# Optimization experiments

Hardware: AMD Instinct MI355X
Metric: run time of the kernel (lower is better)

## Reference

```python
import jax, jax.numpy as jnp
import numpy as np


def _mlp2(x, W1, b1, W2, b2):
    # ReluMLP with two Dense layers: relu between layers, linear output
    return jax.nn.relu(x @ W1 + b1) @ W2 + b2


def setup_inputs() -> dict:
    key = jax.random.key(0)
    N, NP, DIN, D = 100000, 25000, 16, 64
    E, EDS, EP, EUS = 1_600_000, 800_000, 400_000, 200_000
    L = 8  # number of message-passing layers actually used
    ks = iter(jax.random.split(key, 40))
    nrm = lambda shape: jax.random.normal(next(ks), shape, jnp.float32) * 0.05
    ri = lambda n, hi: jax.random.randint(next(ks), (n,), 0, hi)
    return dict(
        x=jax.random.normal(next(ks), (N, DIN), jnp.float32),
        We1=nrm((DIN, D)), be1=jnp.zeros((D,), jnp.float32),
        We2=nrm((D, D)), be2=jnp.zeros((D,), jnp.float32),
        Wm1=nrm((L, D, D)), bm1=jnp.zeros((L, D), jnp.float32),
        Wm2=nrm((L, D, D)), bm2=jnp.zeros((L, D), jnp.float32),
        Wn1=nrm((L, 2 * D, D)), bn1=jnp.zeros((L, D), jnp.float32),
        Wn2=nrm((L, D, D)), bn2=jnp.zeros((L, D), jnp.float32),
        Wd1=nrm((D, D)), bd1=jnp.zeros((D,), jnp.float32),
        Wd2=nrm((D, 2)), bd2=jnp.zeros((2,), jnp.float32),
        s_fine=ri(E, N), r_fine=ri(E, N),
        s_ds=ri(EDS, N), r_ds=ri(EDS, N),
        s_p=ri(EP, NP), r_p=ri(EP, NP),
        s_us=ri(EUS, NP), r_us=ri(EUS, NP),
        uppool=ri(N, NP), downpool=ri(NP, NP),
    )


def reference(x, We1, be1, We2, be2, Wm1, bm1, Wm2, bm2, Wn1, bn1, Wn2, bn2,
              Wd1, bd1, Wd2, bd2, s_fine, r_fine, s_ds, r_ds, s_p, r_p,
              s_us, r_us, uppool, downpool):
    def mp(l, h, s, r, n):
        # LinearMessagePassingLayer: message MLP on sender feats,
        # sum-scatter to receivers (mean_aggr=False), node MLP on [h, aggr]
        msg = _mlp2(h[s], Wm1[l], bm1[l], Wm2[l], bm2[l])          # [E, D]
        aggr = jax.ops.segment_sum(msg, r, num_segments=n)          # [n, D]
        return _mlp2(jnp.concatenate([h, aggr], -1),
                     Wn1[l], bn1[l], Wn2[l], bn2[l])                # [n, D]

    N = x.shape[0]
    NP = downpool.shape[0]
    # encode
    h = _mlp2(x, We1, be1, We2, be2)                                 # [N, D]
    h = mp(0, h, s_fine, r_fine, N)
    h = mp(1, h, s_fine, r_fine, N)
    skip = h
    # Downsample: gather by uppool idx, MP on downsampling graph, select pooled
    g = mp(2, h[uppool], s_ds, r_ds, N)                              # [N, D]
    hp = g[downpool]                                                 # [NP, D]
    # bottleneck
    hp = mp(3, hp, s_p, r_p, NP)
    hp = mp(4, hp, s_p, r_p, NP)
    # Upsample: gather by downpool idx, MP on upsampling graph, select by uppool
    g = mp(5, hp[downpool], s_us, r_us, NP)                          # [NP, D]
    h = g[uppool]                                                    # [N, D]
    # decode with skip connections
    h = mp(6, h, s_fine, r_fine, N) + skip
    h = mp(7, h, s_fine, r_fine, N) + skip
    return _mlp2(h, Wd1, bd1, Wd2, bd2)                              # [N, 2]
```

## Files before the change

kernel.cpp:

```cpp
#include <hip/hip_runtime.h>

#define WG 256

#define MLP_FMA16(ACC, A, W) do { \
    ACC[0][0]=fmaf(A.x,W.x,ACC[0][0]); ACC[0][1]=fmaf(A.x,W.y,ACC[0][1]); \
    ACC[0][2]=fmaf(A.x,W.z,ACC[0][2]); ACC[0][3]=fmaf(A.x,W.w,ACC[0][3]); \
    ACC[1][0]=fmaf(A.y,W.x,ACC[1][0]); ACC[1][1]=fmaf(A.y,W.y,ACC[1][1]); \
    ACC[1][2]=fmaf(A.y,W.z,ACC[1][2]); ACC[1][3]=fmaf(A.y,W.w,ACC[1][3]); \
    ACC[2][0]=fmaf(A.z,W.x,ACC[2][0]); ACC[2][1]=fmaf(A.z,W.y,ACC[2][1]); \
    ACC[2][2]=fmaf(A.z,W.z,ACC[2][2]); ACC[2][3]=fmaf(A.z,W.w,ACC[2][3]); \
    ACC[3][0]=fmaf(A.w,W.x,ACC[3][0]); ACC[3][1]=fmaf(A.w,W.y,ACC[3][1]); \
    ACC[3][2]=fmaf(A.w,W.z,ACC[3][2]); ACC[3][3]=fmaf(A.w,W.w,ACC[3][3]); \
} while (0)

template<int DINA, bool HAS_B, bool HAS_SKIP, bool GATHER_A,
         int MSG_DOUT, bool PARTIAL_MSG, bool WRITE_OUT1>
__global__ __launch_bounds__(WG)
void mlp2_fused(const float* __restrict__ inA, const int* __restrict__ gidxA,
                const float* __restrict__ inB,
                const float* __restrict__ W1, const float* __restrict__ b1,
                const float* __restrict__ W2, const float* __restrict__ b2,
                const float* __restrict__ skip, float* __restrict__ out1,
                const float* __restrict__ M1, const float* __restrict__ mb1,
                const float* __restrict__ M2, const float* __restrict__ mb2,
                float* __restrict__ outM, int msgN, int n)
{
    constexpr int XP = 68;
    __shared__ __align__(16) float sXT[64][XP];
    __shared__ __align__(16) float sW[64 * 64];
    __shared__ float sb[128];
    __shared__ float sW2d[128];
    __shared__ float sb2d[2];

    const int tid = threadIdx.x;
    const int tx = tid & 15, ty = tid >> 4;
    const int c0 = tx * 4, r0 = ty * 4;
    const int row0 = blockIdx.x * 64;
    const int lrow = tid & 63;
    const int kq0 = (tid >> 6) * 4;

    for (int i = tid * 4; i < DINA * 64; i += WG * 4)
        *(float4*)&sW[i] = *(const float4*)&W1[i];
    if (tid < 64) sb[tid] = b1[tid];
    else if (tid < 128) sb[tid] = b2[tid - 64];

    {
        const int rg = min(row0 + lrow, n - 1);
        const int ra = GATHER_A ? gidxA[rg] : rg;
        const float* pA = inA + (size_t)ra * DINA;
        #pragma unroll
        for (int kq = kq0; kq < DINA; kq += 16) {
            const float4 v = *(const float4*)(pA + kq);
            sXT[kq + 0][lrow] = v.x; sXT[kq + 1][lrow] = v.y;
            sXT[kq + 2][lrow] = v.z; sXT[kq + 3][lrow] = v.w;
        }
    }
    __syncthreads();

    float acc[4][4] = {};
    #pragma unroll 8
    for (int k = 0; k < DINA; ++k) {
        const float4 a = *(const float4*)&sXT[k][r0];
        const float4 w = *(const float4*)&sW[k * 64 + c0];
        MLP_FMA16(acc, a, w);
    }

    if constexpr (HAS_B) {
        __syncthreads();
        for (int i = tid * 4; i < 64 * 64; i += WG * 4)
            *(float4*)&sW[i] = *(const float4*)&W1[DINA * 64 + i];
        {
            const int rg = min(row0 + lrow, n - 1);
            const float* pB = inB + (size_t)rg * 64;
            #pragma unroll
            for (int kq = kq0; kq < 64; kq += 16) {
                const float4 v = *(const float4*)(pB + kq);
                sXT[kq + 0][lrow] = v.x; sXT[kq + 1][lrow] = v.y;
                sXT[kq + 2][lrow] = v.z; sXT[kq + 3][lrow] = v.w;
            }
        }
        __syncthreads();
        #pragma unroll 8
        for (int k = 0; k < 64; ++k) {
            const float4 a = *(const float4*)&sXT[k][r0];
            const float4 w = *(const float4*)&sW[k * 64 + c0];
            MLP_FMA16(acc, a, w);
        }
    }
    __syncthreads();

    for (int i = tid * 4; i < 64 * 64; i += WG * 4)
        *(float4*)&sW[i] = *(const float4*)&W2[i];
    #pragma unroll
    for (int j = 0; j < 4; ++j) {
        const float bj = sb[c0 + j];
        *(float4*)&sXT[c0 + j][r0] = make_float4(
            fmaxf(acc[0][j] + bj, 0.f), fmaxf(acc[1][j] + bj, 0.f),
            fmaxf(acc[2][j] + bj, 0.f), fmaxf(acc[3][j] + bj, 0.f));
    }
    __syncthreads();

    float acc2[4][4] = {};
    #pragma unroll 8
    for (int k = 0; k < 64; ++k) {
        const float4 a = *(const float4*)&sXT[k][r0];
        const float4 w = *(const float4*)&sW[k * 64 + c0];
        MLP_FMA16(acc2, a, w);
    }

    float ofull[4][4];
    #pragma unroll
    for (int i = 0; i < 4; ++i) {
        const int row = row0 + r0 + i;
        float4 s = make_float4(0.f, 0.f, 0.f, 0.f);
        if (HAS_SKIP && row < n) s = *(const float4*)&skip[(size_t)row * 64 + c0];
        ofull[i][0] = acc2[i][0] + sb[64 + c0 + 0] + s.x;
        ofull[i][1] = acc2[i][1] + sb[64 + c0 + 1] + s.y;
        ofull[i][2] = acc2[i][2] + sb[64 + c0 + 2] + s.z;
        ofull[i][3] = acc2[i][3] + sb[64 + c0 + 3] + s.w;
        if (WRITE_OUT1 && row < n)
            *(float4*)&out1[(size_t)row * 64 + c0] =
                make_float4(ofull[i][0], ofull[i][1], ofull[i][2], ofull[i][3]);
    }

    if constexpr (MSG_DOUT > 0) {
        if (!PARTIAL_MSG || row0 < msgN) {
            __syncthreads();
            for (int i = tid * 4; i < 64 * 64; i += WG * 4)
                *(float4*)&sW[i] = *(const float4*)&M1[i];
            if constexpr (MSG_DOUT == 64) {
                if (tid < 64) sb[tid] = mb1[tid];
                else if (tid < 128) sb[tid] = mb2[tid - 64];
            } else {
                if (tid < 64) sb[tid] = mb1[tid];
                else if (tid < 192) sW2d[tid - 64] = M2[tid - 64];
                else if (tid < 194) sb2d[tid - 192] = mb2[tid - 192];
            }
            #pragma unroll
            for (int j = 0; j < 4; ++j)
                *(float4*)&sXT[c0 + j][r0] =
                    make_float4(ofull[0][j], ofull[1][j], ofull[2][j], ofull[3][j]);
            __syncthreads();

            float acc3[4][4] = {};
            #pragma unroll 8
            for (int k = 0; k < 64; ++k) {
                const float4 a = *(const float4*)&sXT[k][r0];
                const float4 w = *(const float4*)&sW[k * 64 + c0];
                MLP_FMA16(acc3, a, w);
            }
            __syncthreads();
            if constexpr (MSG_DOUT == 64) {
                for (int i = tid * 4; i < 64 * 64; i += WG * 4)
                    *(float4*)&sW[i] = *(const float4*)&M2[i];
            }
            #pragma unroll
            for (int j = 0; j < 4; ++j) {
                const float bj = sb[c0 + j];
                *(float4*)&sXT[c0 + j][r0] = make_float4(
                    fmaxf(acc3[0][j] + bj, 0.f), fmaxf(acc3[1][j] + bj, 0.f),
                    fmaxf(acc3[2][j] + bj, 0.f), fmaxf(acc3[3][j] + bj, 0.f));
            }
            __syncthreads();

            if constexpr (MSG_DOUT == 64) {
                float accM[4][4] = {};
                #pragma unroll 8
                for (int k = 0; k < 64; ++k) {
                    const float4 a = *(const float4*)&sXT[k][r0];
                    const float4 w = *(const float4*)&sW[k * 64 + c0];
                    MLP_FMA16(accM, a, w);
                }
                #pragma unroll
                for (int i = 0; i < 4; ++i) {
                    const int row = row0 + r0 + i;
                    if (row < msgN)
                        *(float4*)&outM[(size_t)row * 64 + c0] =
                            make_float4(accM[i][0] + sb[64 + c0 + 0],
                                        accM[i][1] + sb[64 + c0 + 1],
                                        accM[i][2] + sb[64 + c0 + 2],
                                        accM[i][3] + sb[64 + c0 + 3]);
                }
            } else {
                if (tid < 128) {
                    const int lr = tid >> 1, col = tid & 1;
                    float o0 = sb2d[col], o1 = 0.0f;
                    #pragma unroll 8
                    for (int k = 0; k < 64; k += 2) {
                        o0 = fmaf(sXT[k][lr],     sW2d[k * 2 + col],       o0);
                        o1 = fmaf(sXT[k + 1][lr], sW2d[(k + 1) * 2 + col], o1);
                    }
                    const int row = row0 + lr;
                    if (row < msgN) outM[(size_t)row * 2 + col] = o0 + o1;
                }
            }
        }
    }
}

template<int DINA, bool HAS_B, bool HAS_SKIP, bool GATHER_A>
__global__ __launch_bounds__(WG)
void mlp2_rt(const float* __restrict__ inA, const int* __restrict__ gidxA,
             const float* __restrict__ inB,
             const float* __restrict__ W1, const float* __restrict__ b1,
             const float* __restrict__ W2, const float* __restrict__ b2,
             const float* __restrict__ skip,
             float* __restrict__ out, int n)
{
    constexpr int XP = 68;
    __shared__ __align__(16) float sXT[64][XP];
    __shared__ __align__(16) float sW[64 * 64];
    __shared__ float sb[128];

    const int tid = threadIdx.x;
    const int tx = tid & 15, ty = tid >> 4;
    const int c0 = tx * 4, r0 = ty * 4;
    const int row0 = blockIdx.x * 64;
    const int lrow = tid & 63;
    const int kq0 = (tid >> 6) * 4;

    for (int i = tid * 4; i < DINA * 64; i += WG * 4)
        *(float4*)&sW[i] = *(const float4*)&W1[i];
    if (tid < 64) sb[tid] = b1[tid];
    else if (tid < 128) sb[tid] = b2[tid - 64];

    {
        const int rg = min(row0 + lrow, n - 1);
        const int ra = GATHER_A ? gidxA[rg] : rg;
        const float* pA = inA + (size_t)ra * DINA;
        #pragma unroll
        for (int kq = kq0; kq < DINA; kq += 16) {
            const float4 v = *(const float4*)(pA + kq);
            sXT[kq + 0][lrow] = v.x; sXT[kq + 1][lrow] = v.y;
            sXT[kq + 2][lrow] = v.z; sXT[kq + 3][lrow] = v.w;
        }
    }
    __syncthreads();

    float acc[4][4] = {};
    #pragma unroll 8
    for (int k = 0; k < DINA; ++k) {
        const float4 a = *(const float4*)&sXT[k][r0];
        const float4 w = *(const float4*)&sW[k * 64 + c0];
        MLP_FMA16(acc, a, w);
    }
    if constexpr (HAS_B) {
        __syncthreads();
        for (int i = tid * 4; i < 64 * 64; i += WG * 4)
            *(float4*)&sW[i] = *(const float4*)&W1[DINA * 64 + i];
        {
            const int rg = min(row0 + lrow, n - 1);
            const float* pB = inB + (size_t)rg * 64;
            #pragma unroll
            for (int kq = kq0; kq < 64; kq += 16) {
                const float4 v = *(const float4*)(pB + kq);
                sXT[kq + 0][lrow] = v.x; sXT[kq + 1][lrow] = v.y;
                sXT[kq + 2][lrow] = v.z; sXT[kq + 3][lrow] = v.w;
            }
        }
        __syncthreads();
        #pragma unroll 8
        for (int k = 0; k < 64; ++k) {
            const float4 a = *(const float4*)&sXT[k][r0];
            const float4 w = *(const float4*)&sW[k * 64 + c0];
            MLP_FMA16(acc, a, w);
        }
    }
    __syncthreads();

    for (int i = tid * 4; i < 64 * 64; i += WG * 4)
        *(float4*)&sW[i] = *(const float4*)&W2[i];
    #pragma unroll
    for (int j = 0; j < 4; ++j) {
        const float bj = sb[c0 + j];
        *(float4*)&sXT[c0 + j][r0] = make_float4(
            fmaxf(acc[0][j] + bj, 0.f), fmaxf(acc[1][j] + bj, 0.f),
            fmaxf(acc[2][j] + bj, 0.f), fmaxf(acc[3][j] + bj, 0.f));
    }
    __syncthreads();

    float acc2[4][4] = {};
    #pragma unroll 8
    for (int k = 0; k < 64; ++k) {
        const float4 a = *(const float4*)&sXT[k][r0];
        const float4 w = *(const float4*)&sW[k * 64 + c0];
        MLP_FMA16(acc2, a, w);
    }
    #pragma unroll
    for (int i = 0; i < 4; ++i) {
        const int row = row0 + r0 + i;
        if (row < n) {
            float4 o = make_float4(acc2[i][0] + sb[64 + c0 + 0],
                                   acc2[i][1] + sb[64 + c0 + 1],
                                   acc2[i][2] + sb[64 + c0 + 2],
                                   acc2[i][3] + sb[64 + c0 + 3]);
            if (HAS_SKIP) {
                const float4 s = *(const float4*)&skip[(size_t)row * 64 + c0];
                o.x += s.x; o.y += s.y; o.z += s.z; o.w += s.w;
            }
            *(float4*)&out[(size_t)row * 64 + c0] = o;
        }
    }
}

__global__ __launch_bounds__(WG)
void fill4_enc_k(const int* __restrict__ s0, const int* __restrict__ r0v, int* cu0, int* sl0, int cap0, int E0, int n0,
                 const int* __restrict__ s1, const int* __restrict__ r1, int* cu1, int* sl1, int cap1, int E1, int n1,
                 const int* __restrict__ s2, const int* __restrict__ r2, int* cu2, int* sl2, int cap2, int E2, int n2,
                 const int* __restrict__ s3, const int* __restrict__ r3, int* cu3, int* sl3, int cap3, int E3, int n3,
                 int W0, int W1n, int W2n, int W3n, int FILLB,
                 const float* __restrict__ x,
                 const float* __restrict__ We1, const float* __restrict__ be1,
                 const float* __restrict__ We2, const float* __restrict__ be2,
                 float* __restrict__ h0,
                 const float* __restrict__ M1, const float* __restrict__ mb1,
                 const float* __restrict__ M2, const float* __restrict__ mb2,
                 float* __restrict__ msg0, int N)
{
    constexpr int XP = 68;
    __shared__ __align__(16) float sXT[64][XP];
    __shared__ float sb[128];

    if ((int)blockIdx.x < FILLB) {
        const int xcd = blockIdx.x & 7;
        int w = blockIdx.x >> 3;
        const int* s; const int* r; int* cur; int* sl; int cap; int E; int n; int W;
        if (w < W0)               { s=s0; r=r0v; cur=cu0; sl=sl0; cap=cap0; E=E0; n=n0; W=W0; }
        else if ((w -= W0) < W1n) { s=s1; r=r1;  cur=cu1; sl=sl1; cap=cap1; E=E1; n=n1; W=W1n; }
        else if ((w -= W1n) < W2n){ s=s2; r=r2;  cur=cu2; sl=sl2; cap=cap2; E=E2; n=n2; W=W2n; }
        else { w -= W2n;            s=s3; r=r3;  cur=cu3; sl=sl3; cap=cap3; E=E3; n=n3; W=W3n; }
        const int lo = (int)(((long)n * xcd) >> 3);
        const int hi = (int)(((long)n * (xcd + 1)) >> 3);
        const int chunk = (E + W - 1) / W;
        const int e0 = w * chunk;
        const int e1 = min(E, e0 + chunk);
        for (int e = e0 + (int)threadIdx.x; e < e1; e += WG) {
            const int v = __builtin_nontemporal_load(&r[e]);
            if (v >= lo && v < hi) {
                const int sv = __builtin_nontemporal_load(&s[e]);
                const int p = atomicAdd(&cur[v], 1);
                if (p < cap) sl[(size_t)v * cap + p] = sv;
            }
        }
        return;
    }

    const int bid = blockIdx.x - FILLB;
    const int tid = threadIdx.x;
    const int tx = tid & 15, ty = tid >> 4;
    const int c0 = tx * 4, r0 = ty * 4;
    const int row0 = bid * 64;
    const int lrow = tid & 63;
    const int kq0 = (tid >> 6) * 4;

    if (tid < 64) sb[tid] = be1[tid];
    else if (tid < 128) sb[tid] = be2[tid - 64];

    {
        const int rg = min(row0 + lrow, N - 1);
        const float* pA = x + (size_t)rg * 16;
        const float4 v = *(const float4*)(pA + kq0);
        sXT[kq0 + 0][lrow] = v.x; sXT[kq0 + 1][lrow] = v.y;
        sXT[kq0 + 2][lrow] = v.z; sXT[kq0 + 3][lrow] = v.w;
    }
    __syncthreads();

    float acc[4][4] = {};
    #pragma unroll
    for (int k = 0; k < 16; ++k) {
        const float4 a = *(const float4*)&sXT[k][r0];
        const float4 w = *(const float4*)&We1[k * 64 + c0];
        MLP_FMA16(acc, a, w);
    }
    __syncthreads();
    #pragma unroll
    for (int j = 0; j < 4; ++j) {
        const float bj = sb[c0 + j];
        *(float4*)&sXT[c0 + j][r0] = make_float4(
            fmaxf(acc[0][j] + bj, 0.f), fmaxf(acc[1][j] + bj, 0.f),
            fmaxf(acc[2][j] + bj, 0.f), fmaxf(acc[3][j] + bj, 0.f));
    }
    __syncthreads();

    float acc2[4][4] = {};
    #pragma unroll 8
    for (int k = 0; k < 64; ++k) {
        const float4 a = *(const float4*)&sXT[k][r0];
        const float4 w = *(const float4*)&We2[k * 64 + c0];
        MLP_FMA16(acc2, a, w);
    }
    float ofull[4][4];
    #pragma unroll
    for (int i = 0; i < 4; ++i) {
        const int row = row0 + r0 + i;
        ofull[i][0] = acc2[i][0] + sb[64 + c0 + 0];
        ofull[i][1] = acc2[i][1] + sb[64 + c0 + 1];
        ofull[i][2] = acc2[i][2] + sb[64 + c0 + 2];
        ofull[i][3] = acc2[i][3] + sb[64 + c0 + 3];
        if (row < N)
            *(float4*)&h0[(size_t)row * 64 + c0] =
                make_float4(ofull[i][0], ofull[i][1], ofull[i][2], ofull[i][3]);
    }

    __syncthreads();
    if (tid < 64) sb[tid] = mb1[tid];
    else if (tid < 128) sb[tid] = mb2[tid - 64];
    #pragma unroll
    for (int j = 0; j < 4; ++j)
        *(float4*)&sXT[c0 + j][r0] =
            make_float4(ofull[0][j], ofull[1][j], ofull[2][j], ofull[3][j]);
    __syncthreads();

    float acc3[4][4] = {};
    #pragma unroll 8
    for (int k = 0; k < 64; ++k) {
        const float4 a = *(const float4*)&sXT[k][r0];
        const float4 w = *(const float4*)&M1[k * 64 + c0];
        MLP_FMA16(acc3, a, w);
    }
    __syncthreads();
    #pragma unroll
    for (int j = 0; j < 4; ++j) {
        const float bj = sb[c0 + j];
        *(float4*)&sXT[c0 + j][r0] = make_float4(
            fmaxf(acc3[0][j] + bj, 0.f), fmaxf(acc3[1][j] + bj, 0.f),
            fmaxf(acc3[2][j] + bj, 0.f), fmaxf(acc3[3][j] + bj, 0.f));
    }
    __syncthreads();

    float accM[4][4] = {};
    #pragma unroll 8
    for (int k = 0; k < 64; ++k) {
        const float4 a = *(const float4*)&sXT[k][r0];
        const float4 w = *(const float4*)&M2[k * 64 + c0];
        MLP_FMA16(accM, a, w);
    }
    #pragma unroll
    for (int i = 0; i < 4; ++i) {
        const int row = row0 + r0 + i;
        if (row < N)
            *(float4*)&msg0[(size_t)row * 64 + c0] =
                make_float4(accM[i][0] + sb[64 + c0 + 0],
                            accM[i][1] + sb[64 + c0 + 1],
                            accM[i][2] + sb[64 + c0 + 2],
                            accM[i][3] + sb[64 + c0 + 3]);
    }
}

template<bool REMAP>
__global__ __launch_bounds__(WG)
void gather_slots_k(const int* __restrict__ deg, const int* __restrict__ slots,
                    int cap, const int* __restrict__ remap,
                    const float* __restrict__ tab, float* __restrict__ aggr, int n)
{
    const int node = blockIdx.x * (WG / 64) + (threadIdx.x >> 6);
    const int c = threadIdx.x & 63;
    if (node >= n) return;
    const int d = min(deg[node], cap);
    const int* sl = slots + (size_t)node * cap;

    int myidx = 0;
    if (c < d) {
        myidx = __builtin_nontemporal_load(&sl[c]);
        if (REMAP) myidx = remap[myidx];
    }

    float a[8] = {};
    int j = 0;
    for (; j + 7 < d; j += 8) {
        #pragma unroll
        for (int u = 0; u < 8; ++u) {
            const int t = __shfl(myidx, j + u);
            a[u] += tab[(size_t)t * 64 + c];
        }
    }
    #pragma unroll 4
    for (; j < d; ++j) {
        const int t = __shfl(myidx, j);
        a[j & 7] += tab[(size_t)t * 64 + c];
    }
    aggr[(size_t)node * 64 + c] =
        ((a[0] + a[1]) + (a[2] + a[3])) + ((a[4] + a[5]) + (a[6] + a[7]));
}

extern "C" void kernel_launch(void* const* d_in, const int* in_sizes, int n_in,
                              void* d_out, int out_size, void* d_ws, size_t ws_size,
                              hipStream_t stream)
{
    const float* x    = (const float*)d_in[0];
    const float* We1  = (const float*)d_in[1];
    const float* be1  = (const float*)d_in[2];
    const float* We2  = (const float*)d_in[3];
    const float* be2  = (const float*)d_in[4];
    const float* Wm1  = (const float*)d_in[5];
    const float* bm1  = (const float*)d_in[6];
    const float* Wm2  = (const float*)d_in[7];
    const float* bm2  = (const float*)d_in[8];
    const float* Wn1  = (const float*)d_in[9];
    const float* bn1  = (const float*)d_in[10];
    const float* Wn2  = (const float*)d_in[11];
    const float* bn2  = (const float*)d_in[12];
    const float* Wd1  = (const float*)d_in[13];
    const float* bd1  = (const float*)d_in[14];
    const float* Wd2  = (const float*)d_in[15];
    const float* bd2  = (const float*)d_in[16];
    const int* s_fine = (const int*)d_in[17];
    const int* r_fine = (const int*)d_in[18];
    const int* s_ds   = (const int*)d_in[19];
    const int* r_ds   = (const int*)d_in[20];
    const int* s_p    = (const int*)d_in[21];
    const int* r_p    = (const int*)d_in[22];
    const int* s_us   = (const int*)d_in[23];
    const int* r_us   = (const int*)d_in[24];
    const int* uppool   = (const int*)d_in[25];
    const int* downpool = (const int*)d_in[26];

    const int N   = in_sizes[0] / 16;
    const int E   = in_sizes[17];
    const int EDS = in_sizes[19];
    const int EP  = in_sizes[21];
    const int EUS = in_sizes[23];
    const int NP  = in_sizes[26];

    const int CAP_FINE = 48, CAP_DS = 32, CAP_PP = 48, CAP_US = 32;

    float* B0  = (float*)d_ws;
    float* B1  = B0 + (size_t)N * 64;
    float* B2  = B1 + (size_t)N * 64;
    float* B3  = B2 + (size_t)N * 64;
    float* HPa = B3 + (size_t)N * 64;
    float* HPb = HPa + (size_t)NP * 64;
    int* ip = (int*)(HPb + (size_t)NP * 64);
    auto alloc_i = [&](size_t n) { int* p = ip; ip += n; return p; };
    int* cur_fine = alloc_i(N);
    int* cur_ds   = alloc_i(N);
    int* cur_pp   = alloc_i(NP);
    int* cur_us   = alloc_i(NP);
    int* sl_fine  = alloc_i((size_t)N * CAP_FINE);
    int* sl_ds    = alloc_i((size_t)N * CAP_DS);
    int* sl_pp    = alloc_i((size_t)NP * CAP_PP);
    int* sl_us    = alloc_i((size_t)NP * CAP_US);

    const int gN  = (N + 63) / 64;
    const int gNP = (NP + 63) / 64;
    const int gaN  = (N + 3) / 4;
    const int gaNP = (NP + 3) / 4;

    hipMemsetAsync(cur_fine, 0, (size_t)(2 * N + 2 * NP) * sizeof(int), stream);
    {
        const int W0 = 256, W1n = 128, W2n = 64, W3n = 64;
        const int FILLB = 8 * (W0 + W1n + W2n + W3n);
        fill4_enc_k<<<FILLB + gN, WG, 0, stream>>>(
            s_fine, r_fine, cur_fine, sl_fine, CAP_FINE, E,   N,
            s_ds,   r_ds,   cur_ds,   sl_ds,   CAP_DS,   EDS, N,
            s_p,    r_p,    cur_pp,   sl_pp,   CAP_PP,   EP,  NP,
            s_us,   r_us,   cur_us,   sl_us,   CAP_US,   EUS, NP,
            W0, W1n, W2n, W3n, FILLB,
            x, We1, be1, We2, be2, B0,
            Wm1 + 0*4096, bm1 + 0*64, Wm2 + 0*4096, bm2 + 0*64, B1, N);
    }
    gather_slots_k<false><<<gaN,WG,0,stream>>>(cur_fine,sl_fine,CAP_FINE,nullptr,B1,B2,N);

    mlp2_fused<64,true,false,false,64,false,true><<<gN,WG,0,stream>>>(
        B0,nullptr,B2, Wn1+0*8192,bn1+0*64,Wn2+0*4096,bn2+0*64, nullptr,B3,
        Wm1+1*4096,bm1+1*64,Wm2+1*4096,bm2+1*64, B0, N, N);
    gather_slots_k<false><<<gaN,WG,0,stream>>>(cur_fine,sl_fine,CAP_FINE,nullptr,B0,B2,N);

    mlp2_fused<64,true,false,false,64,true,true><<<gN,WG,0,stream>>>(
        B3,nullptr,B2, Wn1+1*8192,bn1+1*64,Wn2+1*4096,bn2+1*64, nullptr,B1,
        Wm1+2*4096,bm1+2*64,Wm2+2*4096,bm2+2*64, B0, NP, N);
    gather_slots_k<true><<<gaN,WG,0,stream>>>(cur_ds,sl_ds,CAP_DS,uppool,B0,B2,N);

    mlp2_rt<64,true,false,true><<<gN,WG,0,stream>>>(
        B1,uppool,B2, Wn1+2*8192,bn1+2*64,Wn2+2*4096,bn2+2*64, nullptr,B3,N);

    mlp2_rt<64,false,false,true><<<gNP,WG,0,stream>>>(
        B3,downpool,nullptr, Wm1+3*4096,bm1+3*64,Wm2+3*4096,bm2+3*64, nullptr,HPa,NP);
    gather_slots_k<false><<<gaNP,WG,0,stream>>>(cur_pp,sl_pp,CAP_PP,nullptr,HPa,B2,NP);

    mlp2_fused<64,true,false,true,64,false,true><<<gNP,WG,0,stream>>>(
        B3,downpool,B2, Wn1+3*8192,bn1+3*64,Wn2+3*4096,bn2+3*64, nullptr,HPb,
        Wm1+4*4096,bm1+4*64,Wm2+4*4096,bm2+4*64, HPa, NP, NP);
    gather_slots_k<false><<<gaNP,WG,0,stream>>>(cur_pp,sl_pp,CAP_PP,nullptr,HPa,B2,NP);

    mlp2_fused<64,true,false,false,64,false,true><<<gNP,WG,0,stream>>>(
        HPb,nullptr,B2, Wn1+4*8192,bn1+4*64,Wn2+4*4096,bn2+4*64, nullptr,HPa,
        Wm1+5*4096,bm1+5*64,Wm2+5*4096,bm2+5*64, HPb, NP, NP);
    gather_slots_k<true><<<gaNP,WG,0,stream>>>(cur_us,sl_us,CAP_US,downpool,HPb,B2,NP);

    mlp2_fused<64,true,false,true,64,false,true><<<gNP,WG,0,stream>>>(
        HPa,downpool,B2, Wn1+5*8192,bn1+5*64,Wn2+5*4096,bn2+5*64, nullptr,HPb,
        Wm1+6*4096,bm1+6*64,Wm2+6*4096,bm2+6*64, B3, NP, NP);
    gather_slots_k<true><<<gaN,WG,0,stream>>>(cur_fine,sl_fine,CAP_FINE,uppool,B3,B2,N);

    mlp2_fused<64,true,true,true,64,false,true><<<gN,WG,0,stream>>>(
        HPb,uppool,B2, Wn1+6*8192,bn1+6*64,Wn2+6*4096,bn2+6*64, B1,B0,
        Wm1+7*4096,bm1+7*64,Wm2+7*4096,bm2+7*64, B3, N, N);
    gather_slots_k<false><<<gaN,WG,0,stream>>>(cur_fine,sl_fine,CAP_FINE,nullptr,B3,B2,N);

    mlp2_fused<64,true,true,false,2,false,false><<<gN,WG,0,stream>>>(
        B0,nullptr,B2, Wn1+7*8192,bn1+7*64,Wn2+7*4096,bn2+7*64, B1,nullptr,
        Wd1,bd1,Wd2,bd2, (float*)d_out, N, N);
}
```

Measured before the change: 1.064 ms.

## Spread CSR slot-fill work across later fused MLP kernels to overlap with compute

Before, the first kernel built slot lists for all four graphs. Now it builds only the fine-graph lists. The downsampling graph's fill runs as extra blocks in the first fused MLP launch, and the bottleneck and upsampling fills run in the second, before each list is needed. The fill loop also reads receiver indices as int4 vectors and drops the nontemporal loads, including in gather_slots_k. The aim is to hide fill latency behind MLP compute and shorten the first launch, at the cost of extra grid blocks and branching in the fused MLP kernel.

```diff
diff --git a/kernel.cpp b/kernel.cpp
--- a/kernel.cpp
+++ b/kernel.cpp
@@ -13,6 +13,45 @@
     ACC[3][2]=fmaf(A.w,W.z,ACC[3][2]); ACC[3][3]=fmaf(A.w,W.w,ACC[3][3]); \
 } while (0)
 
+__device__ __forceinline__ void fill_role(int xcd, int w,
+    const int* __restrict__ s, const int* __restrict__ r,
+    int* __restrict__ cur, int* __restrict__ sl,
+    int cap, int E, int n, int W)
+{
+    const int lo = (int)(((long)n * xcd) >> 3);
+    const int hi = (int)(((long)n * (xcd + 1)) >> 3);
+    int chunk = (E + W - 1) / W;
+    chunk = (chunk + 3) & ~3;
+    const int e0 = w * chunk;
+    const int e1 = min(E, e0 + chunk);
+
+    auto fill1 = [&](int v, int e) {
+        if (v >= lo && v < hi) {
+            const int sv = s[e];
+            const int p = atomicAdd(&cur[v], 1);
+            if (p < cap) sl[(size_t)v * cap + p] = sv;
+        }
+    };
+
+    for (int e = e0 + (int)threadIdx.x * 4; e < e1; e += WG * 4) {
+        if (e + 4 <= e1) {
+            const int4 rv = *(const int4*)&r[e];
+            fill1(rv.x, e + 0);
+            fill1(rv.y, e + 1);
+            fill1(rv.z, e + 2);
+            fill1(rv.w, e + 3);
+        } else {
+            for (int j = 0; e + j < e1; ++j) fill1(r[e + j], e + j);
+        }
+    }
+}
+
+struct FillPair {
+    const int* s0; const int* r0; int* cur0; int* sl0; int cap0, E0, n0, W0;
+    const int* s1; const int* r1; int* cur1; int* sl1; int cap1, E1, n1, W1;
+    int FILLB;
+};
+
 template<int DINA, bool HAS_B, bool HAS_SKIP, bool GATHER_A,
          int MSG_DOUT, bool PARTIAL_MSG, bool WRITE_OUT1>
 __global__ __launch_bounds__(WG)
@@ -23,8 +62,19 @@
                 const float* __restrict__ skip, float* __restrict__ out1,
                 const float* __restrict__ M1, const float* __restrict__ mb1,
                 const float* __restrict__ M2, const float* __restrict__ mb2,
-                float* __restrict__ outM, int msgN, int n)
+                float* __restrict__ outM, int msgN, int n, FillPair fa)
 {
+    if (fa.FILLB > 0 && (int)blockIdx.x < fa.FILLB) {
+        const int xcd = blockIdx.x & 7;
+        const int w = blockIdx.x >> 3;
+        if (w < fa.W0)
+            fill_role(xcd, w, fa.s0, fa.r0, fa.cur0, fa.sl0, fa.cap0, fa.E0, fa.n0, fa.W0);
+        else
+            fill_role(xcd, w - fa.W0, fa.s1, fa.r1, fa.cur1, fa.sl1, fa.cap1, fa.E1, fa.n1, fa.W1);
+        return;
+    }
+    const int bid = blockIdx.x - fa.FILLB;
+
     constexpr int XP = 68;
     __shared__ __align__(16) float sXT[64][XP];
     __shared__ __align__(16) float sW[64 * 64];
@@ -35,7 +85,7 @@
     const int tid = threadIdx.x;
     const int tx = tid & 15, ty = tid >> 4;
     const int c0 = tx * 4, r0 = ty * 4;
-    const int row0 = blockIdx.x * 64;
+    const int row0 = bid * 64;
     const int lrow = tid & 63;
     const int kq0 = (tid >> 6) * 4;
 
@@ -304,44 +354,22 @@
 }
 
 __global__ __launch_bounds__(WG)
-void fill4_enc_k(const int* __restrict__ s0, const int* __restrict__ r0v, int* cu0, int* sl0, int cap0, int E0, int n0,
-                 const int* __restrict__ s1, const int* __restrict__ r1, int* cu1, int* sl1, int cap1, int E1, int n1,
-                 const int* __restrict__ s2, const int* __restrict__ r2, int* cu2, int* sl2, int cap2, int E2, int n2,
-                 const int* __restrict__ s3, const int* __restrict__ r3, int* cu3, int* sl3, int cap3, int E3, int n3,
-                 int W0, int W1n, int W2n, int W3n, int FILLB,
-                 const float* __restrict__ x,
-                 const float* __restrict__ We1, const float* __restrict__ be1,
-                 const float* __restrict__ We2, const float* __restrict__ be2,
-                 float* __restrict__ h0,
-                 const float* __restrict__ M1, const float* __restrict__ mb1,
-                 const float* __restrict__ M2, const float* __restrict__ mb2,
-                 float* __restrict__ msg0, int N)
+void fill_enc_k(const int* __restrict__ s0, const int* __restrict__ r0v,
+                int* cu0, int* sl0, int cap0, int E0, int n0, int W0, int FILLB,
+                const float* __restrict__ x,
+                const float* __restrict__ We1, const float* __restrict__ be1,
+                const float* __restrict__ We2, const float* __restrict__ be2,
+                float* __restrict__ h0,
+                const float* __restrict__ M1, const float* __restrict__ mb1,
+                const float* __restrict__ M2, const float* __restrict__ mb2,
+                float* __restrict__ msg0, int N)
 {
     constexpr int XP = 68;
     __shared__ __align__(16) float sXT[64][XP];
     __shared__ float sb[128];
 
     if ((int)blockIdx.x < FILLB) {
-        const int xcd = blockIdx.x & 7;
-        int w = blockIdx.x >> 3;
-        const int* s; const int* r; int* cur; int* sl; int cap; int E; int n; int W;
-        if (w < W0)               { s=s0; r=r0v; cur=cu0; sl=sl0; cap=cap0; E=E0; n=n0; W=W0; }
-        else if ((w -= W0) < W1n) { s=s1; r=r1;  cur=cu1; sl=sl1; cap=cap1; E=E1; n=n1; W=W1n; }
-        else if ((w -= W1n) < W2n){ s=s2; r=r2;  cur=cu2; sl=sl2; cap=cap2; E=E2; n=n2; W=W2n; }
-        else { w -= W2n;            s=s3; r=r3;  cur=cu3; sl=sl3; cap=cap3; E=E3; n=n3; W=W3n; }
-        const int lo = (int)(((long)n * xcd) >> 3);
-        const int hi = (int)(((long)n * (xcd + 1)) >> 3);
-        const int chunk = (E + W - 1) / W;
-        const int e0 = w * chunk;
-        const int e1 = min(E, e0 + chunk);
-        for (int e = e0 + (int)threadIdx.x; e < e1; e += WG) {
-            const int v = __builtin_nontemporal_load(&r[e]);
-            if (v >= lo && v < hi) {
-                const int sv = __builtin_nontemporal_load(&s[e]);
-                const int p = atomicAdd(&cur[v], 1);
-                if (p < cap) sl[(size_t)v * cap + p] = sv;
-            }
-        }
+        fill_role(blockIdx.x & 7, blockIdx.x >> 3, s0, r0v, cu0, sl0, cap0, E0, n0, W0);
         return;
     }
 
@@ -461,7 +489,7 @@
 
     int myidx = 0;
     if (c < d) {
-        myidx = __builtin_nontemporal_load(&sl[c]);
+        myidx = sl[c];
         if (REMAP) myidx = remap[myidx];
     }
 
@@ -546,29 +574,39 @@
     const int gaN  = (N + 3) / 4;
     const int gaNP = (NP + 3) / 4;
 
+    const FillPair fnone = {};
+
     hipMemsetAsync(cur_fine, 0, (size_t)(2 * N + 2 * NP) * sizeof(int), stream);
     {
-        const int W0 = 256, W1n = 128, W2n = 64, W3n = 64;
-        const int FILLB = 8 * (W0 + W1n + W2n + W3n);
-        fill4_enc_k<<<FILLB + gN, WG, 0, stream>>>(
-            s_fine, r_fine, cur_fine, sl_fine, CAP_FINE, E,   N,
-            s_ds,   r_ds,   cur_ds,   sl_ds,   CAP_DS,   EDS, N,
-            s_p,    r_p,    cur_pp,   sl_pp,   CAP_PP,   EP,  NP,
-            s_us,   r_us,   cur_us,   sl_us,   CAP_US,   EUS, NP,
-            W0, W1n, W2n, W3n, FILLB,
+        const int W_FINE = 256;
+        const int FILLB = 8 * W_FINE;
+        fill_enc_k<<<FILLB + gN, WG, 0, stream>>>(
+            s_fine, r_fine, cur_fine, sl_fine, CAP_FINE, E, N, W_FINE, FILLB,
             x, We1, be1, We2, be2, B0,
             Wm1 + 0*4096, bm1 + 0*64, Wm2 + 0*4096, bm2 + 0*64, B1, N);
     }
     gather_slots_k<false><<<gaN,WG,0,stream>>>(cur_fine,sl_fine,CAP_FINE,nullptr,B1,B2,N);
 
-    mlp2_fused<64,true,false,false,64,false,true><<<gN,WG,0,stream>>>(
-        B0,nullptr,B2, Wn1+0*8192,bn1+0*64,Wn2+0*4096,bn2+0*64, nullptr,B3,
-        Wm1+1*4096,bm1+1*64,Wm2+1*4096,bm2+1*64, B0, N, N);
+    {
+        const int W_DS = 128;
+        FillPair fds = { s_ds, r_ds, cur_ds, sl_ds, CAP_DS, EDS, N, W_DS,
+                         nullptr, nullptr, nullptr, nullptr, 0, 0, 0, 0,
+                         8 * W_DS };
+        mlp2_fused<64,true,false,false,64,false,true><<<8*W_DS + gN,WG,0,stream>>>(
+            B0,nullptr,B2, Wn1+0*8192,bn1+0*64,Wn2+0*4096,bn2+0*64, nullptr,B3,
+            Wm1+1*4096,bm1+1*64,Wm2+1*4096,bm2+1*64, B0, N, N, fds);
+    }
     gather_slots_k<false><<<gaN,WG,0,stream>>>(cur_fine,sl_fine,CAP_FINE,nullptr,B0,B2,N);
 
-    mlp2_fused<64,true,false,false,64,true,true><<<gN,WG,0,stream>>>(
-        B3,nullptr,B2, Wn1+1*8192,bn1+1*64,Wn2+1*4096,bn2+1*64, nullptr,B1,
-        Wm1+2*4096,bm1+2*64,Wm2+2*4096,bm2+2*64, B0, NP, N);
+    {
+        const int W_PP = 64, W_US = 32;
+        FillPair fpu = { s_p,  r_p,  cur_pp, sl_pp, CAP_PP, EP,  NP, W_PP,
+                         s_us, r_us, cur_us, sl_us, CAP_US, EUS, NP, W_US,
+                         8 * (W_PP + W_US) };
+        mlp2_fused<64,true,false,false,64,true,true><<<8*(W_PP+W_US) + gN,WG,0,stream>>>(
+            B3,nullptr,B2, Wn1+1*8192,bn1+1*64,Wn2+1*4096,bn2+1*64, nullptr,B1,
+            Wm1+2*4096,bm1+2*64,Wm2+2*4096,bm2+2*64, B0, NP, N, fpu);
+    }
     gather_slots_k<true><<<gaN,WG,0,stream>>>(cur_ds,sl_ds,CAP_DS,uppool,B0,B2,N);
 
     mlp2_rt<64,true,false,true><<<gN,WG,0,stream>>>(
@@ -580,25 +618,25 @@
 
     mlp2_fused<64,true,false,true,64,false,true><<<gNP,WG,0,stream>>>(
         B3,downpool,B2, Wn1+3*8192,bn1+3*64,Wn2+3*4096,bn2+3*64, nullptr,HPb,
-        Wm1+4*4096,bm1+4*64,Wm2+4*4096,bm2+4*64, HPa, NP, NP);
+        Wm1+4*4096,bm1+4*64,Wm2+4*4096,bm2+4*64, HPa, NP, NP, fnone);
     gather_slots_k<false><<<gaNP,WG,0,stream>>>(cur_pp,sl_pp,CAP_PP,nullptr,HPa,B2,NP);
 
     mlp2_fused<64,true,false,false,64,false,true><<<gNP,WG,0,stream>>>(
         HPb,nullptr,B2, Wn1+4*8192,bn1+4*64,Wn2+4*4096,bn2+4*64, nullptr,HPa,
-        Wm1+5*4096,bm1+5*64,Wm2+5*4096,bm2+5*64, HPb, NP, NP);
+        Wm1+5*4096,bm1+5*64,Wm2+5*4096,bm2+5*64, HPb, NP, NP, fnone);
     gather_slots_k<true><<<gaNP,WG,0,stream>>>(cur_us,sl_us,CAP_US,downpool,HPb,B2,NP);
 
     mlp2_fused<64,true,false,true,64,false,true><<<gNP,WG,0,stream>>>(
         HPa,downpool,B2, Wn1+5*8192,bn1+5*64,Wn2+5*4096,bn2+5*64, nullptr,HPb,
-        Wm1+6*4096,bm1+6*64,Wm2+6*4096,bm2+6*64, B3, NP, NP);
+        Wm1+6*4096,bm1+6*64,Wm2+6*4096,bm2+6*64, B3, NP, NP, fnone);
     gather_slots_k<true><<<gaN,WG,0,stream>>>(cur_fine,sl_fine,CAP_FINE,uppool,B3,B2,N);
 
     mlp2_fused<64,true,true,true,64,false,true><<<gN,WG,0,stream>>>(
         HPb,uppool,B2, Wn1+6*8192,bn1+6*64,Wn2+6*4096,bn2+6*64, B1,B0,
-        Wm1+7*4096,bm1+7*64,Wm2+7*4096,bm2+7*64, B3, N, N);
+        Wm1+7*4096,bm1+7*64,Wm2+7*4096,bm2+7*64, B3, N, N, fnone);
     gather_slots_k<false><<<gaN,WG,0,stream>>>(cur_fine,sl_fine,CAP_FINE,nullptr,B3,B2,N);
 
     mlp2_fused<64,true,true,false,2,false,false><<<gN,WG,0,stream>>>(
         B0,nullptr,B2, Wn1+7*8192,bn1+7*64,Wn2+7*4096,bn2+7*64, B1,nullptr,
-        Wd1,bd1,Wd2,bd2, (float*)d_out, N, N);
+        Wd1,bd1,Wd2,bd2, (float*)d_out, N, N, fnone);
 }
```

Result: faster. 988.1 us (-7.1%).
